# Optimization experiments

Measured on AMD Instinct MI355X. Metric: run time of the kernel, lower is better.

The kernel has to match this reference:

```python
import jax, jax.numpy as jnp
import numpy as np

K_V = 0.5
G_OFF = 0.001
G_ON = 0.005
N_IN = 4096
N_OUT = 4096
BATCH = 8192


def setup_inputs() -> dict:
    key = jax.random.key(0)
    k1, k2, k3 = jax.random.split(key, 3)
    x = jax.random.normal(k1, (BATCH, N_IN), dtype=jnp.float32)
    # RandomNormal(stddev=1/sqrt(neurons_in)) initializer
    w = jax.random.normal(k2, (N_IN, N_OUT), dtype=jnp.float32) / np.sqrt(N_IN)
    # bias initialized to 0 in the module; use small noise so it is non-degenerate
    b = jax.random.normal(k3, (N_OUT,), dtype=jnp.float32) * 0.01
    return {"x": x, "w": w, "b": b}


def reference(x, w, b):
    # combine_weights: fold bias as an extra input row, x gets a ones column
    weights = jnp.concatenate([w, b[None, :]], axis=0)            # (n_in+1, n_out)
    ones = jnp.ones((x.shape[0], 1), dtype=x.dtype)
    voltages = K_V * jnp.concatenate([x, ones], axis=1)           # (B, n_in+1)

    # weights_to_conductances, 'lowest' mapping rule (differential pair)
    max_weight = jnp.max(jnp.abs(weights))
    k_cond = (G_ON - G_OFF) / max_weight
    g_eff = k_cond * weights
    g_pos = G_OFF + jnp.maximum(g_eff, 0.0)                       # even columns
    g_neg = G_OFF - jnp.minimum(g_eff, 0.0)                       # odd columns
    # interleave pos/neg -> (n_in+1, 2*n_out)
    conductances = jnp.stack([g_pos, g_neg], axis=-1).reshape(weights.shape[0], -1)

    # crossbar currents: scaled GEMM
    currents = voltages @ conductances                            # (B, 2*n_out)

    # differential current subtraction + rescale back to weight domain
    total_currents = currents[:, 0::2] - currents[:, 1::2]        # (B, n_out)
    y_disturbed = total_currents / (K_V * k_cond)
    return y_disturbed
```

## Files before the change

### kernel.cpp

```cpp
#include <hip/hip_runtime.h>
#include <cstdint>

typedef unsigned short u16;
typedef __attribute__((ext_vector_type(8))) __bf16 bf16x8;
typedef __attribute__((ext_vector_type(4))) float f32x4;

#define M_DIM 8192
#define N_DIM 4096
#define K_DIM 4096

#define CVT_X_BLOCKS 16384
#define CVT_W_BLOCKS 4096

__device__ __forceinline__ u16 f2bf(float f) {
    union { float f; uint32_t u; } v; v.f = f;
    uint32_t u = v.u;
    u += 0x7FFFu + ((u >> 16) & 1u);
    return (u16)(u >> 16);
}

__global__ __launch_bounds__(256) void cvt_kernel(const float* __restrict__ x,
                                                  const float* __restrict__ w,
                                                  u16* __restrict__ xb,
                                                  u16* __restrict__ wt) {
    const int t = threadIdx.x;
    if (blockIdx.x < CVT_X_BLOCKS) {
        size_t i = ((size_t)blockIdx.x * 256 + t) * 8;
        const float4* p = (const float4*)(x + i);
        float4 v0 = p[0], v1 = p[1];
        uint32_t o0 = (uint32_t)f2bf(v0.x) | ((uint32_t)f2bf(v0.y) << 16);
        uint32_t o1 = (uint32_t)f2bf(v0.z) | ((uint32_t)f2bf(v0.w) << 16);
        uint32_t o2 = (uint32_t)f2bf(v1.x) | ((uint32_t)f2bf(v1.y) << 16);
        uint32_t o3 = (uint32_t)f2bf(v1.z) | ((uint32_t)f2bf(v1.w) << 16);
        uint4 o; o.x = o0; o.y = o1; o.z = o2; o.w = o3;
        *(uint4*)(xb + i) = o;
    } else {
        __shared__ u16 lds[64 * 68];
        const int bid = blockIdx.x - CVT_X_BLOCKS;
        const int k0 = (bid & 63) * 64;
        const int n0 = (bid >> 6) * 64;
#pragma unroll
        for (int i = 0; i < 4; ++i) {
            int idx = i * 256 + t;
            int r = idx >> 4;
            int c4 = (idx & 15) * 4;
            float4 v = *(const float4*)&w[(size_t)(k0 + r) * N_DIM + n0 + c4];
            uint2 o;
            o.x = (uint32_t)f2bf(v.x) | ((uint32_t)f2bf(v.y) << 16);
            o.y = (uint32_t)f2bf(v.z) | ((uint32_t)f2bf(v.w) << 16);
            *(uint2*)&lds[r * 68 + c4] = o;
        }
        __syncthreads();
#pragma unroll
        for (int i = 0; i < 4; ++i) {
            int idx = i * 256 + t;
            int rn  = idx >> 4;
            int ck  = (idx & 15) * 4;
            uint2 o;
            o.x = (uint32_t)lds[(ck + 0) * 68 + rn] | ((uint32_t)lds[(ck + 1) * 68 + rn] << 16);
            o.y = (uint32_t)lds[(ck + 2) * 68 + rn] | ((uint32_t)lds[(ck + 3) * 68 + rn] << 16);
            *(uint2*)&wt[(size_t)(n0 + rn) * K_DIM + k0 + ck] = o;
        }
    }
}

typedef const uint32_t __attribute__((address_space(1)))* gp_t;
typedef uint32_t __attribute__((address_space(3)))* lp_t;

__global__ __launch_bounds__(256) void gemm_kernel(const u16* __restrict__ A,
                                                   const u16* __restrict__ Bt,
                                                   const float* __restrict__ bias,
                                                   float* __restrict__ C) {
    __shared__ u16 As[128 * 32];
    __shared__ u16 Bs[128 * 32];

    const int t    = threadIdx.x;
    const int lane = t & 63;
    const int l16  = lane & 15;
    const int quad = lane >> 4;
    const int wave = t >> 6;
    const int wm   = (wave >> 1) * 64;
    const int wn   = (wave & 1) * 64;
    const int bm   = blockIdx.y * 128;
    const int bn   = blockIdx.x * 128;

    f32x4 acc[4][4] = {};

    const int c0 = t, c1 = 256 + t;
    const int rA0 = c0 >> 2, rA1 = c1 >> 2;
    const int sw  = ((rA0 >> 1) & 3);
    const int kc  = ((c0 & 3) ^ sw) * 8;
    const u16* a0 = A  + (size_t)(bm + rA0) * K_DIM + kc;
    const u16* a1 = A  + (size_t)(bm + rA1) * K_DIM + kc;
    const u16* b0 = Bt + (size_t)(bn + rA0) * K_DIM + kc;
    const u16* b1 = Bt + (size_t)(bn + rA1) * K_DIM + kc;

    const int sw8 = (quad ^ ((l16 >> 1) & 3)) * 8;

    for (int k0 = 0; k0 < K_DIM; k0 += 32) {
        __syncthreads();
        __builtin_amdgcn_global_load_lds((gp_t)(a0 + k0), (lp_t)&As[c0 * 8], 16, 0, 0);
        __builtin_amdgcn_global_load_lds((gp_t)(a1 + k0), (lp_t)&As[c1 * 8], 16, 0, 0);
        __builtin_amdgcn_global_load_lds((gp_t)(b0 + k0), (lp_t)&Bs[c0 * 8], 16, 0, 0);
        __builtin_amdgcn_global_load_lds((gp_t)(b1 + k0), (lp_t)&Bs[c1 * 8], 16, 0, 0);
        __syncthreads();

        bf16x8 af[4], bf[4];
#pragma unroll
        for (int i = 0; i < 4; ++i) {
            af[i] = *(const bf16x8*)&As[(wm + i * 16 + l16) * 32 + sw8];
            bf[i] = *(const bf16x8*)&Bs[(wn + i * 16 + l16) * 32 + sw8];
        }
#pragma unroll
        for (int i = 0; i < 4; ++i)
#pragma unroll
            for (int j = 0; j < 4; ++j)
                acc[i][j] = __builtin_amdgcn_mfma_f32_16x16x32_bf16(af[i], bf[j], acc[i][j], 0, 0, 0);
    }

#pragma unroll
    for (int j = 0; j < 4; ++j) {
        const int col = bn + wn + j * 16 + l16;
        const float bv = bias[col];
#pragma unroll
        for (int i = 0; i < 4; ++i) {
            const int row = bm + wm + i * 16 + quad * 4;
#pragma unroll
            for (int r = 0; r < 4; ++r)
                C[(size_t)(row + r) * N_DIM + col] = acc[i][j][r] + bv;
        }
    }
}

extern "C" void kernel_launch(void* const* d_in, const int* in_sizes, int n_in,
                              void* d_out, int out_size, void* d_ws, size_t ws_size,
                              hipStream_t stream) {
    const float* x = (const float*)d_in[0];
    const float* w = (const float*)d_in[1];
    const float* b = (const float*)d_in[2];
    float* out = (float*)d_out;

    u16* xb = (u16*)d_ws;
    u16* wt = xb + (size_t)M_DIM * K_DIM;

    cvt_kernel<<<CVT_X_BLOCKS + CVT_W_BLOCKS, 256, 0, stream>>>(x, w, xb, wt);
    gemm_kernel<<<dim3(N_DIM / 128, M_DIM / 128), 256, 0, stream>>>(xb, wt, b, out);
}
```

Before: 566.4 us.

## Add dedicated loader wave and double-buffered LDS to overlap loads with MFMA

The GEMM block grows from four to five waves. The fifth wave only issues global-to-LDS loads into a two-stage buffer, and the other four waves run MFMA compute on the stage that is already loaded. Loading tile k+1 while tile k is being computed, with one barrier per K-step instead of two, is meant to hide global load latency. The costs are that one wave must now issue all 16 loads per step, the LDS footprint doubles, and correctness relies on the loads being waited on before each barrier.

```diff
diff --git a/kernel.cpp b/kernel.cpp
--- a/kernel.cpp
+++ b/kernel.cpp
@@ -8,6 +8,7 @@
 #define M_DIM 8192
 #define N_DIM 4096
 #define K_DIM 4096
+#define NK    (K_DIM / 32)
 
 #define CVT_X_BLOCKS 16384
 #define CVT_W_BLOCKS 4096
@@ -28,11 +29,11 @@
         size_t i = ((size_t)blockIdx.x * 256 + t) * 8;
         const float4* p = (const float4*)(x + i);
         float4 v0 = p[0], v1 = p[1];
-        uint32_t o0 = (uint32_t)f2bf(v0.x) | ((uint32_t)f2bf(v0.y) << 16);
-        uint32_t o1 = (uint32_t)f2bf(v0.z) | ((uint32_t)f2bf(v0.w) << 16);
-        uint32_t o2 = (uint32_t)f2bf(v1.x) | ((uint32_t)f2bf(v1.y) << 16);
-        uint32_t o3 = (uint32_t)f2bf(v1.z) | ((uint32_t)f2bf(v1.w) << 16);
-        uint4 o; o.x = o0; o.y = o1; o.z = o2; o.w = o3;
+        uint4 o;
+        o.x = (uint32_t)f2bf(v0.x) | ((uint32_t)f2bf(v0.y) << 16);
+        o.y = (uint32_t)f2bf(v0.z) | ((uint32_t)f2bf(v0.w) << 16);
+        o.z = (uint32_t)f2bf(v1.x) | ((uint32_t)f2bf(v1.y) << 16);
+        o.w = (uint32_t)f2bf(v1.z) | ((uint32_t)f2bf(v1.w) << 16);
         *(uint4*)(xb + i) = o;
     } else {
         __shared__ u16 lds[64 * 68];
@@ -42,8 +43,7 @@
 #pragma unroll
         for (int i = 0; i < 4; ++i) {
             int idx = i * 256 + t;
-            int r = idx >> 4;
-            int c4 = (idx & 15) * 4;
+            int r = idx >> 4, c4 = (idx & 15) * 4;
             float4 v = *(const float4*)&w[(size_t)(k0 + r) * N_DIM + n0 + c4];
             uint2 o;
             o.x = (uint32_t)f2bf(v.x) | ((uint32_t)f2bf(v.y) << 16);
@@ -54,8 +54,7 @@
 #pragma unroll
         for (int i = 0; i < 4; ++i) {
             int idx = i * 256 + t;
-            int rn  = idx >> 4;
-            int ck  = (idx & 15) * 4;
+            int rn = idx >> 4, ck = (idx & 15) * 4;
             uint2 o;
             o.x = (uint32_t)lds[(ck + 0) * 68 + rn] | ((uint32_t)lds[(ck + 1) * 68 + rn] << 16);
             o.y = (uint32_t)lds[(ck + 2) * 68 + rn] | ((uint32_t)lds[(ck + 3) * 68 + rn] << 16);
@@ -67,67 +66,86 @@
 typedef const uint32_t __attribute__((address_space(1)))* gp_t;
 typedef uint32_t __attribute__((address_space(3)))* lp_t;
 
-__global__ __launch_bounds__(256) void gemm_kernel(const u16* __restrict__ A,
+__global__ __launch_bounds__(320) void gemm_kernel(const u16* __restrict__ A,
                                                    const u16* __restrict__ Bt,
                                                    const float* __restrict__ bias,
                                                    float* __restrict__ C) {
-    __shared__ u16 As[128 * 32];
-    __shared__ u16 Bs[128 * 32];
+    __shared__ u16 As[2][128 * 32];
+    __shared__ u16 Bs[2][128 * 32];
 
     const int t    = threadIdx.x;
     const int lane = t & 63;
-    const int l16  = lane & 15;
-    const int quad = lane >> 4;
     const int wave = t >> 6;
-    const int wm   = (wave >> 1) * 64;
-    const int wn   = (wave & 1) * 64;
     const int bm   = blockIdx.y * 128;
     const int bn   = blockIdx.x * 128;
 
-    f32x4 acc[4][4] = {};
+    if (wave == 4) {
+        const int q  = lane >> 2;
+        const int kc = ((lane & 3) ^ ((lane >> 3) & 3)) * 8;
+        const u16* pa[8];
+        const u16* pb[8];
+#pragma unroll
+        for (int j = 0; j < 8; ++j) {
+            pa[j] = A  + (size_t)(bm + j * 16 + q) * K_DIM + kc;
+            pb[j] = Bt + (size_t)(bn + j * 16 + q) * K_DIM + kc;
+        }
+        const int ldst = lane * 8;
+#pragma unroll
+        for (int j = 0; j < 8; ++j) {
+            __builtin_amdgcn_global_load_lds((gp_t)(pa[j]), (lp_t)&As[0][j * 512 + ldst], 16, 0, 0);
+            __builtin_amdgcn_global_load_lds((gp_t)(pb[j]), (lp_t)&Bs[0][j * 512 + ldst], 16, 0, 0);
+        }
+        __syncthreads();
+        for (int k = 0; k < NK; ++k) {
+            if (k + 1 < NK) {
+                const int koff = (k + 1) * 32;
+                const int nb = (k + 1) & 1;
+#pragma unroll
+                for (int j = 0; j < 8; ++j) {
+                    __builtin_amdgcn_global_load_lds((gp_t)(pa[j] + koff), (lp_t)&As[nb][j * 512 + ldst], 16, 0, 0);
+                    __builtin_amdgcn_global_load_lds((gp_t)(pb[j] + koff), (lp_t)&Bs[nb][j * 512 + ldst], 16, 0, 0);
+                }
+            }
+            __syncthreads();
+        }
+    } else {
+        const int l16  = lane & 15;
+        const int quad = lane >> 4;
+        const int wm   = (wave >> 1) * 64;
+        const int wn   = (wave & 1) * 64;
+        const int sw8  = (quad ^ ((l16 >> 1) & 3)) * 8;
 
-    const int c0 = t, c1 = 256 + t;
-    const int rA0 = c0 >> 2, rA1 = c1 >> 2;
-    const int sw  = ((rA0 >> 1) & 3);
-    const int kc  = ((c0 & 3) ^ sw) * 8;
-    const u16* a0 = A  + (size_t)(bm + rA0) * K_DIM + kc;
-    const u16* a1 = A  + (size_t)(bm + rA1) * K_DIM + kc;
-    const u16* b0 = Bt + (size_t)(bn + rA0) * K_DIM + kc;
-    const u16* b1 = Bt + (size_t)(bn + rA1) * K_DIM + kc;
+        f32x4 acc[4][4] = {};
 
-    const int sw8 = (quad ^ ((l16 >> 1) & 3)) * 8;
-
-    for (int k0 = 0; k0 < K_DIM; k0 += 32) {
         __syncthreads();
-        __builtin_amdgcn_global_load_lds((gp_t)(a0 + k0), (lp_t)&As[c0 * 8], 16, 0, 0);
-        __builtin_amdgcn_global_load_lds((gp_t)(a1 + k0), (lp_t)&As[c1 * 8], 16, 0, 0);
-        __builtin_amdgcn_global_load_lds((gp_t)(b0 + k0), (lp_t)&Bs[c0 * 8], 16, 0, 0);
-        __builtin_amdgcn_global_load_lds((gp_t)(b1 + k0), (lp_t)&Bs[c1 * 8], 16, 0, 0);
-        __syncthreads();
-
-        bf16x8 af[4], bf[4];
+        for (int k = 0; k < NK; ++k) {
+            const u16* as = As[k & 1];
+            const u16* bs = Bs[k & 1];
+            bf16x8 af[4], bf[4];
 #pragma unroll
-        for (int i = 0; i < 4; ++i) {
-            af[i] = *(const bf16x8*)&As[(wm + i * 16 + l16) * 32 + sw8];
-            bf[i] = *(const bf16x8*)&Bs[(wn + i * 16 + l16) * 32 + sw8];
+            for (int i = 0; i < 4; ++i) {
+                af[i] = *(const bf16x8*)&as[(wm + i * 16 + l16) * 32 + sw8];
+                bf[i] = *(const bf16x8*)&bs[(wn + i * 16 + l16) * 32 + sw8];
+            }
+#pragma unroll
+            for (int i = 0; i < 4; ++i)
+#pragma unroll
+                for (int j = 0; j < 4; ++j)
+                    acc[i][j] = __builtin_amdgcn_mfma_f32_16x16x32_bf16(af[i], bf[j], acc[i][j], 0, 0, 0);
+            __syncthreads();
         }
-#pragma unroll
-        for (int i = 0; i < 4; ++i)
-#pragma unroll
-            for (int j = 0; j < 4; ++j)
-                acc[i][j] = __builtin_amdgcn_mfma_f32_16x16x32_bf16(af[i], bf[j], acc[i][j], 0, 0, 0);
-    }
 
 #pragma unroll
-    for (int j = 0; j < 4; ++j) {
-        const int col = bn + wn + j * 16 + l16;
-        const float bv = bias[col];
+        for (int j = 0; j < 4; ++j) {
+            const int col = bn + wn + j * 16 + l16;
+            const float bv = bias[col];
 #pragma unroll
-        for (int i = 0; i < 4; ++i) {
-            const int row = bm + wm + i * 16 + quad * 4;
+            for (int i = 0; i < 4; ++i) {
+                const int row = bm + wm + i * 16 + quad * 4;
 #pragma unroll
-            for (int r = 0; r < 4; ++r)
-                C[(size_t)(row + r) * N_DIM + col] = acc[i][j][r] + bv;
+                for (int r = 0; r < 4; ++r)
+                    C[(size_t)(row + r) * N_DIM + col] = acc[i][j][r] + bv;
+            }
         }
     }
 }
@@ -144,5 +162,5 @@
     u16* wt = xb + (size_t)M_DIM * K_DIM;
 
     cvt_kernel<<<CVT_X_BLOCKS + CVT_W_BLOCKS, 256, 0, stream>>>(x, w, xb, wt);
-    gemm_kernel<<<dim3(N_DIM / 128, M_DIM / 128), 256, 0, stream>>>(xb, wt, b, out);
+    gemm_kernel<<<dim3(N_DIM / 128, M_DIM / 128), 320, 0, stream>>>(xb, wt, b, out);
 }
```

Result: slower. 676.4 us (+19.4%).
